# Kernel tuning notes

Measured on AMD Instinct MI355X. Metric: run time of the kernel, lower is better.

Reference implementation:

```python
import jax, jax.numpy as jnp
import numpy as np

NUM_HEADS = 12


def setup_inputs() -> dict:
    key = jax.random.key(0)
    ks = jax.random.split(key, 6)
    dim = 384
    B, N = 2048, 49
    nW = 64
    return {
        "x": jax.random.normal(ks[0], (B, N, dim), dtype=jnp.float32),
        "mask": jax.random.normal(ks[1], (nW, N, N), dtype=jnp.float32),
        "qkv_w": jax.random.normal(ks[2], (3 * dim, dim), dtype=jnp.float32) * 0.02,
        "qkv_b": jax.random.normal(ks[3], (3 * dim,), dtype=jnp.float32) * 0.02,
        "proj_w": jax.random.normal(ks[4], (dim, dim), dtype=jnp.float32) * 0.02,
        "proj_b": jax.random.normal(ks[5], (dim,), dtype=jnp.float32) * 0.02,
    }


def reference(x, mask, qkv_w, qkv_b, proj_w, proj_b):
    B, N, C = x.shape
    H = NUM_HEADS
    Dh = C // H
    scale = Dh ** -0.5
    nW = mask.shape[0]

    # qkv projection: [B, N, 3C]
    qkv = x @ qkv_w.T + qkv_b
    q, k, v = jnp.split(qkv, 3, axis=-1)

    def heads(t):  # [B, N, C] -> [B, H, N, Dh]
        return t.reshape(B, N, H, Dh).transpose(0, 2, 1, 3)

    q, k, v = heads(q) * scale, heads(k), heads(v)

    # [B, H, N, N] attention scores
    attn = jnp.einsum("bhnd,bhmd->bhnm", q, k)
    # add per-window additive mask: reshape B -> (B//nW, nW)
    attn = attn.reshape(B // nW, nW, H, N, N) + mask[None, :, None, :, :]
    attn = jax.nn.softmax(attn.reshape(B, H, N, N), axis=-1)

    out = jnp.einsum("bhnm,bhmd->bhnd", attn, v)
    out = out.transpose(0, 2, 1, 3).reshape(B, N, C)
    return out @ proj_w.T + proj_b
```

## Files before the change

### kernel.cpp

```cpp
#include <hip/hip_runtime.h>
#include <hip/hip_bf16.h>
#include <stdint.h>

typedef unsigned short u16;
typedef __attribute__((ext_vector_type(8))) short short8;
typedef __attribute__((ext_vector_type(4))) float f32x4;

__device__ inline u16 f2bf(float f) {
    union { float f; unsigned int u; } x; x.f = f;
    unsigned int u = x.u;
    unsigned int r = (u + 0x7FFFu + ((u >> 16) & 1u)) >> 16;
    return (u16)r;
}

__device__ inline void gld_lds16(const u16* g, u16* l) {
    auto const* gp = reinterpret_cast<const __attribute__((address_space(1))) unsigned int*>(
        reinterpret_cast<uintptr_t>(g));
    auto* lp = reinterpret_cast<__attribute__((address_space(3))) unsigned int*>(
        reinterpret_cast<uintptr_t>(l));
    __builtin_amdgcn_global_load_lds(gp, lp, 16, 0, 0);
}

#define NX8 4816896
#define NQ8 55296
#define NP8 18432
__global__ __launch_bounds__(256) void prep_all(const float* __restrict__ x,
                                                const float* __restrict__ qw,
                                                const float* __restrict__ pw,
                                                u16* __restrict__ xb,
                                                u16* __restrict__ wq,
                                                u16* __restrict__ wp) {
    size_t i = (size_t)blockIdx.x * 256 + threadIdx.x;
    const float* src; u16* dst; size_t off;
    if (i < NX8)            { src = x;  dst = xb; off = i; }
    else if (i < NX8 + NQ8) { src = qw; dst = wq; off = i - NX8; }
    else                    { src = pw; dst = wp; off = i - (NX8 + NQ8); }
    float4 v0 = ((const float4*)src)[off * 2];
    float4 v1 = ((const float4*)src)[off * 2 + 1];
    u16 h[8];
    h[0] = f2bf(v0.x); h[1] = f2bf(v0.y); h[2] = f2bf(v0.z); h[3] = f2bf(v0.w);
    h[4] = f2bf(v1.x); h[5] = f2bf(v1.y); h[6] = f2bf(v1.z); h[7] = f2bf(v1.w);
    *(uint4*)(dst + off * 8) = *(const uint4*)h;
}

__global__ __launch_bounds__(256) void qkv_gemm(const u16* __restrict__ xb,
                                                const u16* __restrict__ wq,
                                                const float* __restrict__ bias,
                                                u16* __restrict__ qkv_out) {
    __shared__ u16 As[128 * 32];
    __shared__ u16 Bs[128 * 32];
    const int tid = threadIdx.x;
    const int wave = tid >> 6, lane = tid & 63;
    const int lr = lane >> 4, lc = lane & 15;
    const int wm = (wave & 1) * 64, wn = (wave >> 1) * 64;
    const int lin = blockIdx.x;
    const int xcd = lin & 7;
    const int idx = lin >> 3;
    const int nBase = (idx % 9) * 128;
    const int mBase = (xcd * 98 + idx / 9) * 128;

    f32x4 acc[4][4] = {};

    const int srow = lane >> 2, scol = (lane & 3) * 8;
    const u16* aSrc = xb + (size_t)(mBase + wave * 32 + srow) * 384 + scol;
    const u16* bSrc = wq + (size_t)(nBase + wave * 32 + srow) * 384 + scol;
    u16* aDst = &As[wave * 1024];
    u16* bDst = &Bs[wave * 1024];

    for (int k0 = 0; k0 < 384; k0 += 32) {
        gld_lds16(aSrc + k0, aDst);
        gld_lds16(aSrc + k0 + (size_t)16 * 384, aDst + 512);
        gld_lds16(bSrc + k0, bDst);
        gld_lds16(bSrc + k0 + (size_t)16 * 384, bDst + 512);
        __syncthreads();
        short8 af[4], bfr[4];
#pragma unroll
        for (int i = 0; i < 4; ++i)
            af[i] = *(const short8*)&As[(wm + i * 16 + lc) * 32 + lr * 8];
#pragma unroll
        for (int j = 0; j < 4; ++j)
            bfr[j] = *(const short8*)&Bs[(wn + j * 16 + lc) * 32 + lr * 8];
#pragma unroll
        for (int i = 0; i < 4; ++i)
#pragma unroll
            for (int j = 0; j < 4; ++j)
                acc[i][j] = __builtin_amdgcn_mfma_f32_16x16x32_bf16(bfr[j], af[i], acc[i][j], 0, 0, 0);
        __syncthreads();
    }

    const float scale = 0.17677669529663687f;
#pragma unroll
    for (int j = 0; j < 4; ++j) {
        int gnb = nBase + wn + j * 16 + lr * 4;
        float4 bv = *(const float4*)&bias[gnb];
        float mult = (gnb < 384) ? scale : 1.0f;
#pragma unroll
        for (int i = 0; i < 4; ++i) {
            int gm = mBase + wm + i * 16 + lc;
            union { u16 h[4]; uint2 u; } pk;
            pk.h[0] = f2bf((acc[i][j][0] + bv.x) * mult);
            pk.h[1] = f2bf((acc[i][j][1] + bv.y) * mult);
            pk.h[2] = f2bf((acc[i][j][2] + bv.z) * mult);
            pk.h[3] = f2bf((acc[i][j][3] + bv.w) * mult);
            *(uint2*)(qkv_out + (size_t)gm * 1152 + gnb) = pk.u;
        }
    }
}

#define PST 68
__global__ __launch_bounds__(256, 3) void attn_kernel(const u16* __restrict__ qkv,
                                                      const float* __restrict__ mask,
                                                      u16* __restrict__ aout) {
    __shared__ u16 P_s[4][64 * PST];
    __shared__ u16 Vt_s[4][32 * PST];
    const int tid = threadIdx.x;
    const int wave = tid >> 6, lane = tid & 63;
    const int lr = lane >> 4, lc = lane & 15;
    const int bid = blockIdx.x;
    const int b = bid / 3;
    const int h = (bid - b * 3) * 4 + wave;
    const int w = b & 63;
    const float* mrow = mask + (size_t)w * 2401;

    const u16* Q = qkv + (size_t)b * 49 * 1152 + h * 32;
    const u16* K = Q + 384;
    const u16* V = Q + 768;

    {
        u16 vv[32];
        if (lane < 49) {
#pragma unroll
            for (int c = 0; c < 4; ++c)
                *(uint4*)&vv[c * 8] = *(const uint4*)(V + (size_t)lane * 1152 + c * 8);
        } else {
#pragma unroll
            for (int c = 0; c < 32; ++c) vv[c] = 0;
        }
#pragma unroll
        for (int d = 0; d < 32; ++d)
            Vt_s[wave][d * PST + lane] = vv[d];
    }

    short8 qf[4], kf[4];
    const short8 z8 = {0, 0, 0, 0, 0, 0, 0, 0};
#pragma unroll
    for (int i = 0; i < 4; ++i) {
        int row = i * 16 + lc;
        qf[i] = (row < 49) ? *(const short8*)(Q + (size_t)row * 1152 + lr * 8) : z8;
        kf[i] = (row < 49) ? *(const short8*)(K + (size_t)row * 1152 + lr * 8) : z8;
    }
    __syncthreads();

    f32x4 S[4][4] = {};
#pragma unroll
    for (int i = 0; i < 4; ++i)
#pragma unroll
        for (int j = 0; j < 4; ++j)
            S[i][j] = __builtin_amdgcn_mfma_f32_16x16x32_bf16(qf[i], kf[j], S[i][j], 0, 0, 0);

    float l_sum[4][4];
#pragma unroll
    for (int si = 0; si < 4; ++si) {
#pragma unroll
        for (int r = 0; r < 4; ++r) {
            int i = si * 16 + lr * 4 + r;
            int im = (i < 49) ? i : 48;
            float s = 0.0f;
#pragma unroll
            for (int sj = 0; sj < 4; ++sj) {
                int jc = sj * 16 + lc;
                float t = (jc < 49) ? (S[si][sj][r] + mrow[im * 49 + jc]) : -1e30f;
                float p = __expf(t);
                s += p;
                S[si][sj][r] = p;
            }
            s += __shfl_xor(s, 1);
            s += __shfl_xor(s, 2);
            s += __shfl_xor(s, 4);
            s += __shfl_xor(s, 8);
            l_sum[si][r] = s;
        }
    }

#pragma unroll
    for (int si = 0; si < 4; ++si)
#pragma unroll
        for (int sj = 0; sj < 4; ++sj)
#pragma unroll
            for (int r = 0; r < 4; ++r) {
                int i = si * 16 + lr * 4 + r;
                int jc = sj * 16 + lc;
                P_s[wave][i * PST + jc] = f2bf(S[si][sj][r]);
            }
    __syncthreads();

    short8 vf[2][2];
#pragma unroll
    for (int nt = 0; nt < 2; ++nt)
#pragma unroll
        for (int kt = 0; kt < 2; ++kt)
            vf[nt][kt] = *(const short8*)&Vt_s[wave][(nt * 16 + lc) * PST + kt * 32 + lr * 8];

    f32x4 O[4][2] = {};
#pragma unroll
    for (int si = 0; si < 4; ++si) {
#pragma unroll
        for (int kt = 0; kt < 2; ++kt) {
            short8 pf = *(const short8*)&P_s[wave][(si * 16 + lc) * PST + kt * 32 + lr * 8];
#pragma unroll
            for (int nt = 0; nt < 2; ++nt)
                O[si][nt] = __builtin_amdgcn_mfma_f32_16x16x32_bf16(pf, vf[nt][kt], O[si][nt], 0, 0, 0);
        }
    }

#pragma unroll
    for (int si = 0; si < 4; ++si) {
#pragma unroll
        for (int nt = 0; nt < 2; ++nt) {
#pragma unroll
            for (int r = 0; r < 4; ++r) {
                int i = si * 16 + lr * 4 + r;
                if (i < 49) {
                    float val = O[si][nt][r] * __builtin_amdgcn_rcpf(l_sum[si][r]);
                    aout[(size_t)(b * 49 + i) * 384 + h * 32 + nt * 16 + lc] = f2bf(val);
                }
            }
        }
    }
}

__global__ __launch_bounds__(256) void proj_gemm(const u16* __restrict__ a,
                                                 const u16* __restrict__ wp,
                                                 const float* __restrict__ bias,
                                                 float* __restrict__ out) {
    __shared__ u16 As[128 * 32];
    __shared__ u16 Bs[128 * 32];
    const int tid = threadIdx.x;
    const int wave = tid >> 6, lane = tid & 63;
    const int lr = lane >> 4, lc = lane & 15;
    const int wm = (wave & 1) * 64, wn = (wave >> 1) * 64;
    const int lin = blockIdx.x;
    const int xcd = lin & 7;
    const int idx = lin >> 3;
    const int nBase = (idx % 3) * 128;
    const int mBase = (xcd * 98 + idx / 3) * 128;

    f32x4 acc[4][4] = {};

    const int srow = lane >> 2, scol = (lane & 3) * 8;
    const u16* aSrc = a  + (size_t)(mBase + wave * 32 + srow) * 384 + scol;
    const u16* bSrc = wp + (size_t)(nBase + wave * 32 + srow) * 384 + scol;
    u16* aDst = &As[wave * 1024];
    u16* bDst = &Bs[wave * 1024];

    for (int k0 = 0; k0 < 384; k0 += 32) {
        gld_lds16(aSrc + k0, aDst);
        gld_lds16(aSrc + k0 + (size_t)16 * 384, aDst + 512);
        gld_lds16(bSrc + k0, bDst);
        gld_lds16(bSrc + k0 + (size_t)16 * 384, bDst + 512);
        __syncthreads();
        short8 af[4], bfr[4];
#pragma unroll
        for (int i = 0; i < 4; ++i)
            af[i] = *(const short8*)&As[(wm + i * 16 + lc) * 32 + lr * 8];
#pragma unroll
        for (int j = 0; j < 4; ++j)
            bfr[j] = *(const short8*)&Bs[(wn + j * 16 + lc) * 32 + lr * 8];
#pragma unroll
        for (int i = 0; i < 4; ++i)
#pragma unroll
            for (int j = 0; j < 4; ++j)
                acc[i][j] = __builtin_amdgcn_mfma_f32_16x16x32_bf16(bfr[j], af[i], acc[i][j], 0, 0, 0);
        __syncthreads();
    }

#pragma unroll
    for (int j = 0; j < 4; ++j) {
        int gnb = nBase + wn + j * 16 + lr * 4;
        float4 bv = *(const float4*)&bias[gnb];
#pragma unroll
        for (int i = 0; i < 4; ++i) {
            int gm = mBase + wm + i * 16 + lc;
            float4 o;
            o.x = acc[i][j][0] + bv.x;
            o.y = acc[i][j][1] + bv.y;
            o.z = acc[i][j][2] + bv.z;
            o.w = acc[i][j][3] + bv.w;
            *(float4*)(out + (size_t)gm * 384 + gnb) = o;
        }
    }
}

extern "C" void kernel_launch(void* const* d_in, const int* in_sizes, int n_in,
                              void* d_out, int out_size, void* d_ws, size_t ws_size,
                              hipStream_t stream) {
    const float* x      = (const float*)d_in[0];
    const float* mask   = (const float*)d_in[1];
    const float* qkv_w  = (const float*)d_in[2];
    const float* qkv_b  = (const float*)d_in[3];
    const float* proj_w = (const float*)d_in[4];
    const float* proj_b = (const float*)d_in[5];
    float* out = (float*)d_out;

    char* ws = (char*)d_ws;
    u16* wq   = (u16*)ws;
    u16* wp   = (u16*)(ws + 884736);
    u16* qkvb = (u16*)(ws + 884736 + 294912);
    u16* xb   = (u16*)(ws + 884736 + 294912 + 231211008);
    u16* attn = xb;

    prep_all<<<19104, 256, 0, stream>>>(x, qkv_w, proj_w, xb, wq, wp);
    qkv_gemm<<<7056, 256, 0, stream>>>(xb, wq, qkv_b, qkvb);
    attn_kernel<<<6144, 256, 0, stream>>>(qkvb, mask, attn);
    proj_gemm<<<2352, 256, 0, stream>>>(attn, wp, proj_b, out);
}
```

Before: 595.5 us.

## Compute transposed scores so P stays in registers for PV MFMA

Computes S^T (K·Q^T) so that each lane holds probabilities along the key dimension in the layout a 16x16x16 bf16 MFMA expects as its B operand. This feeds P directly from registers into the PV product instead of staging it through shared memory. It removes the P_s LDS buffer, its writes and reads, and one __syncthreads, which lowers LDS use and may allow higher occupancy. The cost is more, smaller MFMAs for PV, mask reads that are now strided per lane, and an inline-asm fallback for the MFMA builtin.

```diff
diff --git a/kernel.cpp b/kernel.cpp
--- a/kernel.cpp
+++ b/kernel.cpp
@@ -4,6 +4,7 @@
 
 typedef unsigned short u16;
 typedef __attribute__((ext_vector_type(8))) short short8;
+typedef __attribute__((ext_vector_type(4))) short s4v;
 typedef __attribute__((ext_vector_type(4))) float f32x4;
 
 __device__ inline u16 f2bf(float f) {
@@ -20,6 +21,19 @@
         reinterpret_cast<uintptr_t>(l));
     __builtin_amdgcn_global_load_lds(gp, lp, 16, 0, 0);
 }
+
+#if __has_builtin(__builtin_amdgcn_mfma_f32_16x16x16bf16_1k)
+#define MFMA16(a, b, c) __builtin_amdgcn_mfma_f32_16x16x16bf16_1k((a), (b), (c), 0, 0, 0)
+#elif __has_builtin(__builtin_amdgcn_mfma_f32_16x16x16_bf16)
+#define MFMA16(a, b, c) __builtin_amdgcn_mfma_f32_16x16x16_bf16((a), (b), (c), 0, 0, 0)
+#else
+__device__ inline f32x4 mfma16_asm(s4v a, s4v b, f32x4 c) {
+    asm volatile("s_nop 1\n\tv_mfma_f32_16x16x16_bf16 %0, %1, %2, %0\n\ts_nop 7\n\ts_nop 7"
+                 : "+v"(c) : "v"(a), "v"(b));
+    return c;
+}
+#define MFMA16(a, b, c) mfma16_asm((a), (b), (c))
+#endif
 
 #define NX8 4816896
 #define NQ8 55296
@@ -107,11 +121,10 @@
     }
 }
 
-#define PST 68
 __global__ __launch_bounds__(256, 3) void attn_kernel(const u16* __restrict__ qkv,
                                                       const float* __restrict__ mask,
                                                       u16* __restrict__ aout) {
-    __shared__ u16 P_s[4][64 * PST];
+#define PST 68
     __shared__ u16 Vt_s[4][32 * PST];
     const int tid = threadIdx.x;
     const int wave = tid >> 6, lane = tid & 63;
@@ -149,84 +162,67 @@
         qf[i] = (row < 49) ? *(const short8*)(Q + (size_t)row * 1152 + lr * 8) : z8;
         kf[i] = (row < 49) ? *(const short8*)(K + (size_t)row * 1152 + lr * 8) : z8;
     }
+
     __syncthreads();
 
-    f32x4 S[4][4] = {};
-#pragma unroll
-    for (int i = 0; i < 4; ++i)
-#pragma unroll
-        for (int j = 0; j < 4; ++j)
-            S[i][j] = __builtin_amdgcn_mfma_f32_16x16x32_bf16(qf[i], kf[j], S[i][j], 0, 0, 0);
-
-    float l_sum[4][4];
+    s4v vfA[2][4];
+#pragma unroll
+    for (int nt = 0; nt < 2; ++nt)
+#pragma unroll
+        for (int sj = 0; sj < 4; ++sj)
+            vfA[nt][sj] = *(const s4v*)&Vt_s[wave][(nt * 16 + lc) * PST + sj * 16 + lr * 4];
+
+    f32x4 S2[4][4] = {};
+#pragma unroll
+    for (int si = 0; si < 4; ++si)
+#pragma unroll
+        for (int sj = 0; sj < 4; ++sj)
+            S2[si][sj] = __builtin_amdgcn_mfma_f32_16x16x32_bf16(kf[sj], qf[si], S2[si][sj], 0, 0, 0);
+
+    const size_t orow = (size_t)b * 49 * 384 + h * 32 + lr * 4;
 #pragma unroll
     for (int si = 0; si < 4; ++si) {
-#pragma unroll
-        for (int r = 0; r < 4; ++r) {
-            int i = si * 16 + lr * 4 + r;
-            int im = (i < 49) ? i : 48;
-            float s = 0.0f;
-#pragma unroll
-            for (int sj = 0; sj < 4; ++sj) {
-                int jc = sj * 16 + lc;
-                float t = (jc < 49) ? (S[si][sj][r] + mrow[im * 49 + jc]) : -1e30f;
+        int q = si * 16 + lc;
+        int im = (q < 49) ? q : 48;
+        const float* mq = mrow + im * 49;
+        float s = 0.0f;
+        s4v pfq[4];
+#pragma unroll
+        for (int sj = 0; sj < 4; ++sj) {
+            int kbase = sj * 16 + lr * 4;
+            s4v pk;
+#pragma unroll
+            for (int r = 0; r < 4; ++r) {
+                int k = kbase + r;
+                float t = (k < 49) ? (S2[si][sj][r] + mq[k]) : -1e30f;
                 float p = __expf(t);
                 s += p;
-                S[si][sj][r] = p;
+                pk[r] = (short)f2bf(p);
             }
-            s += __shfl_xor(s, 1);
-            s += __shfl_xor(s, 2);
-            s += __shfl_xor(s, 4);
-            s += __shfl_xor(s, 8);
-            l_sum[si][r] = s;
-        }
-    }
-
-#pragma unroll
-    for (int si = 0; si < 4; ++si)
-#pragma unroll
-        for (int sj = 0; sj < 4; ++sj)
-#pragma unroll
-            for (int r = 0; r < 4; ++r) {
-                int i = si * 16 + lr * 4 + r;
-                int jc = sj * 16 + lc;
-                P_s[wave][i * PST + jc] = f2bf(S[si][sj][r]);
-            }
-    __syncthreads();
-
-    short8 vf[2][2];
-#pragma unroll
-    for (int nt = 0; nt < 2; ++nt)
-#pragma unroll
-        for (int kt = 0; kt < 2; ++kt)
-            vf[nt][kt] = *(const short8*)&Vt_s[wave][(nt * 16 + lc) * PST + kt * 32 + lr * 8];
-
-    f32x4 O[4][2] = {};
-#pragma unroll
-    for (int si = 0; si < 4; ++si) {
-#pragma unroll
-        for (int kt = 0; kt < 2; ++kt) {
-            short8 pf = *(const short8*)&P_s[wave][(si * 16 + lc) * PST + kt * 32 + lr * 8];
-#pragma unroll
-            for (int nt = 0; nt < 2; ++nt)
-                O[si][nt] = __builtin_amdgcn_mfma_f32_16x16x32_bf16(pf, vf[nt][kt], O[si][nt], 0, 0, 0);
-        }
-    }
-
-#pragma unroll
-    for (int si = 0; si < 4; ++si) {
-#pragma unroll
-        for (int nt = 0; nt < 2; ++nt) {
-#pragma unroll
-            for (int r = 0; r < 4; ++r) {
-                int i = si * 16 + lr * 4 + r;
-                if (i < 49) {
-                    float val = O[si][nt][r] * __builtin_amdgcn_rcpf(l_sum[si][r]);
-                    aout[(size_t)(b * 49 + i) * 384 + h * 32 + nt * 16 + lc] = f2bf(val);
-                }
-            }
-        }
-    }
+            pfq[sj] = pk;
+        }
+        s += __shfl_xor(s, 16);
+        s += __shfl_xor(s, 32);
+
+        f32x4 O0 = {}, O1 = {};
+#pragma unroll
+        for (int sj = 0; sj < 4; ++sj) {
+            O0 = MFMA16(vfA[0][sj], pfq[sj], O0);
+            O1 = MFMA16(vfA[1][sj], pfq[sj], O1);
+        }
+
+        if (q < 49) {
+            float rl = __builtin_amdgcn_rcpf(s);
+            union { u16 h[4]; uint2 u; } pk;
+            pk.h[0] = f2bf(O0[0] * rl); pk.h[1] = f2bf(O0[1] * rl);
+            pk.h[2] = f2bf(O0[2] * rl); pk.h[3] = f2bf(O0[3] * rl);
+            *(uint2*)(aout + orow + (size_t)q * 384) = pk.u;
+            pk.h[0] = f2bf(O1[0] * rl); pk.h[1] = f2bf(O1[1] * rl);
+            pk.h[2] = f2bf(O1[2] * rl); pk.h[3] = f2bf(O1[3] * rl);
+            *(uint2*)(aout + orow + (size_t)q * 384 + 16) = pk.u;
+        }
+    }
+#undef PST
 }
 
 __global__ __launch_bounds__(256) void proj_gemm(const u16* __restrict__ a,
@@ -305,8 +301,8 @@
     char* ws = (char*)d_ws;
     u16* wq   = (u16*)ws;
     u16* wp   = (u16*)(ws + 884736);
-    u16* qkvb = (u16*)(ws + 884736 + 294912);
-    u16* xb   = (u16*)(ws + 884736 + 294912 + 231211008);
+    u16* qkvb = (u16*)(ws + 1179648);
+    u16* xb   = (u16*)(ws + 232390656);
     u16* attn = xb;
 
     prep_all<<<19104, 256, 0, stream>>>(x, qkv_w, proj_w, xb, wq, wp);
```

Measured after the change: 570.1 us. 4.3% less time.
